# Kernel tuning notes

Hardware: AMD Instinct MI355X
Metric: run time of the kernel (lower is better)

## Reference

```python
import jax, jax.numpy as jnp
import numpy as np

B, S, H = 8, 2048, 1024  # batch, sqi_dim, hidden_dim


def setup_inputs() -> dict:
    key = jax.random.key(0)
    ks = jax.random.split(key, 10)
    lim_h = 1.0 / np.sqrt(H)
    lim_1 = 1.0  # Linear(1, H): fan_in = 1
    return {
        "hidden_states": jax.random.normal(ks[0], (B, S, H), dtype=jnp.float32),
        "sqi_sequence": jax.random.uniform(ks[1], (B, 1, S), dtype=jnp.float32),
        "pos_enc": jnp.zeros((1, S, H), dtype=jnp.float32),
        "Wq": jax.random.uniform(ks[2], (H, H), minval=-lim_h, maxval=lim_h),
        "bq": jax.random.uniform(ks[3], (H,), minval=-lim_h, maxval=lim_h),
        "Wk": jax.random.uniform(ks[4], (H, 1), minval=-lim_1, maxval=lim_1),
        "bk": jax.random.uniform(ks[5], (H,), minval=-lim_1, maxval=lim_1),
        "Wv": jax.random.uniform(ks[6], (H, H), minval=-lim_h, maxval=lim_h),
        "bv": jax.random.uniform(ks[7], (H,), minval=-lim_h, maxval=lim_h),
    }


def reference(hidden_states, sqi_sequence, pos_enc, Wq, bq, Wk, bk, Wv, bv):
    # hidden_states: [B, S, H]; sqi_sequence: [B, 1, S]
    x = hidden_states + pos_enc[:, :S, :]
    q = jnp.einsum("bsh,oh->bso", x, Wq) + bq                     # [B, S, H]
    sqi = jnp.transpose(sqi_sequence, (0, 2, 1))                   # [B, S, 1]
    k = sqi * Wk[:, 0] + bk                                        # Linear(1->H): [B, S, H]
    v = jnp.einsum("bsh,oh->bso", x, Wv) + bv                     # [B, S, H]
    scores = jnp.einsum("bqh,bkh->bqk", q, k) / jnp.sqrt(jnp.float32(H))
    attn = jax.nn.softmax(scores, axis=-1)                         # dropout = identity (eval)
    out = jnp.einsum("bqk,bkh->bqh", attn, v)                      # [B, S, H]
    context = jnp.mean(out, axis=1)                                # [B, H]
    return context, attn
```

## Files before the change

### kernel.cpp

```cpp
#include <hip/hip_runtime.h>
#include <math.h>

#define Bq 8
#define Sq 2048
#define Hq 1024
#define QT 8
#define INV_SQRT_H (1.0f / 32.0f)

typedef float f32x4 __attribute__((ext_vector_type(4)));

__device__ __forceinline__ float waveReduceSum(float v) {
#pragma unroll
    for (int off = 32; off > 0; off >>= 1) v += __shfl_xor(v, off, 64);
    return v;
}

__global__ void k_prep(const float* __restrict__ Wq, const float* __restrict__ Wk,
                       const float* __restrict__ bq, const float* __restrict__ sqi,
                       float* __restrict__ wq_eff, float* __restrict__ cb,
                       float* __restrict__ ext) {
    int bid = blockIdx.x, t = threadIdx.x;
    int wid = t >> 6, lane = t & 63;
    if (bid < 256) {
        int hc = bid & 3, oc = bid >> 2;
        int h = hc * 256 + t, o0 = oc * 16;
        float acc = 0.f;
#pragma unroll
        for (int o = 0; o < 16; ++o)
            acc += Wq[(size_t)(o0 + o) * Hq + h] * Wk[o0 + o];
        atomicAdd(&wq_eff[h], acc);
    } else if (bid == 256) {
        float acc = 0.f;
#pragma unroll
        for (int j = 0; j < 4; ++j) acc += bq[t * 4 + j] * Wk[t * 4 + j];
        acc = waveReduceSum(acc);
        __shared__ float red[4];
        if (lane == 0) red[wid] = acc;
        __syncthreads();
        if (t == 0) *cb = (red[0] + red[1] + red[2] + red[3]) * INV_SQRT_H;
    } else {
        int b = bid - 257;
        float mn = 1e30f, mx = -1e30f;
        for (int j = t; j < Sq; j += 256) {
            float v = sqi[b * Sq + j];
            mn = fminf(mn, v);
            mx = fmaxf(mx, v);
        }
#pragma unroll
        for (int off = 32; off > 0; off >>= 1) {
            mn = fminf(mn, __shfl_xor(mn, off, 64));
            mx = fmaxf(mx, __shfl_xor(mx, off, 64));
        }
        __shared__ float smn[4], smx[4];
        if (lane == 0) { smn[wid] = mn; smx[wid] = mx; }
        __syncthreads();
        if (t == 0) {
            ext[b]      = fminf(fminf(smn[0], smn[1]), fminf(smn[2], smn[3]));
            ext[Bq + b] = fmaxf(fmaxf(smx[0], smx[1]), fmaxf(smx[2], smx[3]));
        }
    }
}

__global__ void __launch_bounds__(256) k_attn(
        const float* __restrict__ hidden, const float* __restrict__ pos,
        const float* __restrict__ wq_eff, const float* __restrict__ cbp,
        const float* __restrict__ sqi, const float* __restrict__ ext,
        float* __restrict__ attn, float* __restrict__ wcol) {
    int b = blockIdx.y, qt = blockIdx.x, t = threadIdx.x;
    int wid = t >> 6, lane = t & 63;
    __shared__ float sqi_s[Sq];
    __shared__ float colsum[Sq];
    {
        const float4* sp = (const float4*)(sqi + b * Sq);
        float4* ds = (float4*)sqi_s;
        ds[t]       = sp[t];
        ds[256 + t] = sp[256 + t];
        float4* cz = (float4*)colsum;
        cz[t]       = make_float4(0.f, 0.f, 0.f, 0.f);
        cz[256 + t] = make_float4(0.f, 0.f, 0.f, 0.f);
    }
    float smin = ext[b], smax = ext[Bq + b];
    float cbv = *cbp;

    const float4* wp = (const float4*)wq_eff;
    float4 w0 = wp[lane], w1 = wp[lane + 64], w2 = wp[lane + 128], w3 = wp[lane + 192];
    int q0 = qt * QT + wid * 2;
    float a[2];
#pragma unroll
    for (int r = 0; r < 2; ++r) {
        const float4* hp = (const float4*)(hidden + (size_t)(b * Sq + q0 + r) * Hq);
        const float4* pp = (const float4*)(pos + (size_t)(q0 + r) * Hq);
        float4 h0 = hp[lane], h1 = hp[lane + 64], h2 = hp[lane + 128], h3 = hp[lane + 192];
        float4 p0 = pp[lane], p1 = pp[lane + 64], p2 = pp[lane + 128], p3 = pp[lane + 192];
        float d = (h0.x + p0.x) * w0.x + (h0.y + p0.y) * w0.y + (h0.z + p0.z) * w0.z + (h0.w + p0.w) * w0.w
                + (h1.x + p1.x) * w1.x + (h1.y + p1.y) * w1.y + (h1.z + p1.z) * w1.z + (h1.w + p1.w) * w1.w
                + (h2.x + p2.x) * w2.x + (h2.y + p2.y) * w2.y + (h2.z + p2.z) * w2.z + (h2.w + p2.w) * w2.w
                + (h3.x + p3.x) * w3.x + (h3.y + p3.y) * w3.y + (h3.z + p3.z) * w3.z + (h3.w + p3.w) * w3.w;
        d = waveReduceSum(d);
        a[r] = d * INV_SQRT_H + cbv;
    }
    __syncthreads();

    const float4* ss = (const float4*)sqi_s;
    float4 ca[8];
#pragma unroll
    for (int c = 0; c < 8; ++c) ca[c] = make_float4(0.f, 0.f, 0.f, 0.f);

#pragma unroll
    for (int r = 0; r < 2; ++r) {
        float aa = a[r];
        float m = (aa > 0.f) ? aa * smax : aa * smin;
        float4 e[8];
        float s = 0.f;
#pragma unroll
        for (int c = 0; c < 8; ++c) {
            float4 sv = ss[lane + 64 * c];
            e[c].x = __expf(aa * sv.x - m);
            e[c].y = __expf(aa * sv.y - m);
            e[c].z = __expf(aa * sv.z - m);
            e[c].w = __expf(aa * sv.w - m);
            s += e[c].x + e[c].y + e[c].z + e[c].w;
        }
        s = waveReduceSum(s);
        float rinv = 1.0f / s;
        f32x4* orow = (f32x4*)(attn + (size_t)(b * Sq + q0 + r) * Sq);
#pragma unroll
        for (int c = 0; c < 8; ++c) {
            f32x4 p;
            p.x = e[c].x * rinv; p.y = e[c].y * rinv;
            p.z = e[c].z * rinv; p.w = e[c].w * rinv;
            __builtin_nontemporal_store(p, &orow[lane + 64 * c]);
            ca[c].x += p.x; ca[c].y += p.y; ca[c].z += p.z; ca[c].w += p.w;
        }
    }

#pragma unroll
    for (int c = 0; c < 8; ++c) {
        int base = (lane + 64 * c) * 4;
        atomicAdd(&colsum[base + 0], ca[c].x);
        atomicAdd(&colsum[base + 1], ca[c].y);
        atomicAdd(&colsum[base + 2], ca[c].z);
        atomicAdd(&colsum[base + 3], ca[c].w);
    }
    __syncthreads();
#pragma unroll
    for (int j = 0; j < 8; ++j)
        atomicAdd(&wcol[b * Sq + j * 256 + t], colsum[j * 256 + t]);
}

__global__ void k_y(const float* __restrict__ hidden, const float* __restrict__ pos,
                    const float* __restrict__ wcol, float* __restrict__ y) {
    int b = blockIdx.y, kc = blockIdx.x, t = threadIdx.x;
    int kk0 = kc * 32;
    float4 acc = {0, 0, 0, 0};
#pragma unroll 8
    for (int i = 0; i < 32; ++i) {
        int kk = kk0 + i;
        float wv = wcol[b * Sq + kk] * (1.0f / Sq);
        float4 hv = ((const float4*)(hidden + ((size_t)(b * Sq + kk)) * Hq))[t];
        float4 pv = ((const float4*)(pos + (size_t)kk * Hq))[t];
        acc.x += wv * (hv.x + pv.x);
        acc.y += wv * (hv.y + pv.y);
        acc.z += wv * (hv.z + pv.z);
        acc.w += wv * (hv.w + pv.w);
    }
    atomicAdd(&y[b * Hq + t * 4 + 0], acc.x);
    atomicAdd(&y[b * Hq + t * 4 + 1], acc.y);
    atomicAdd(&y[b * Hq + t * 4 + 2], acc.z);
    atomicAdd(&y[b * Hq + t * 4 + 3], acc.w);
}

__global__ void k_ctx(const float* __restrict__ Wv, const float* __restrict__ bv,
                      const float* __restrict__ y, float* __restrict__ ctx) {
    int b = blockIdx.y, t = threadIdx.x;
    int wid = t >> 6, lane = t & 63;
    __shared__ float4 ys4[Hq / 4];
    ys4[t] = ((const float4*)(y + b * Hq))[t];
    __syncthreads();
    float4 y0 = ys4[lane], y1 = ys4[lane + 64], y2 = ys4[lane + 128], y3 = ys4[lane + 192];
    int h0 = blockIdx.x * 16 + wid * 4;
#pragma unroll
    for (int r = 0; r < 4; ++r) {
        int h = h0 + r;
        const float4* wrow = (const float4*)(Wv + (size_t)h * Hq);
        float4 v0 = wrow[lane], v1 = wrow[lane + 64], v2 = wrow[lane + 128], v3 = wrow[lane + 192];
        float d = v0.x * y0.x + v0.y * y0.y + v0.z * y0.z + v0.w * y0.w
                + v1.x * y1.x + v1.y * y1.y + v1.z * y1.z + v1.w * y1.w
                + v2.x * y2.x + v2.y * y2.y + v2.z * y2.z + v2.w * y2.w
                + v3.x * y3.x + v3.y * y3.y + v3.z * y3.z + v3.w * y3.w;
        d = waveReduceSum(d);
        if (lane == 0) ctx[b * Hq + h] = d + bv[h];
    }
}

extern "C" void kernel_launch(void* const* d_in, const int* in_sizes, int n_in,
                              void* d_out, int out_size, void* d_ws, size_t ws_size,
                              hipStream_t stream) {
    const float* hidden = (const float*)d_in[0];
    const float* sqi    = (const float*)d_in[1];
    const float* pos    = (const float*)d_in[2];
    const float* Wq     = (const float*)d_in[3];
    const float* bq     = (const float*)d_in[4];
    const float* Wk     = (const float*)d_in[5];
    const float* Wv     = (const float*)d_in[7];
    const float* bv     = (const float*)d_in[8];

    float* out  = (float*)d_out;
    float* ctx  = out;
    float* attn = out + Bq * Hq;

    float* ws     = (float*)d_ws;
    float* wq_eff = ws;
    float* wcol   = ws + 1024;
    float* y      = ws + 17408;
    float* ext    = ws + 25600;
    float* cb     = ws + 25616;

    (void)hipMemsetAsync(ws, 0, 25600 * sizeof(float), stream);

    k_prep<<<265, 256, 0, stream>>>(Wq, Wk, bq, sqi, wq_eff, cb, ext);
    k_attn<<<dim3(Sq / QT, Bq), 256, 0, stream>>>(hidden, pos, wq_eff, cb,
                                                  sqi, ext, attn, wcol);
    k_y   <<<dim3(64, Bq), 256, 0, stream>>>(hidden, pos, wcol, y);
    k_ctx <<<dim3(Hq / 16, Bq), 256, 0, stream>>>(Wv, bv, y, ctx);
}
```

Measured before the change: 307.6 us.

## Split attention into row-stats, column-sum, and pure-write kernels

Splits the fused attention kernel into three. The first computes each row's score scale and softmax normaliser. The second recomputes the exponentials in column order to form the column sums of attn without shared or global atomics per element. The third recomputes the probabilities and only streams the attn matrix out, with 16 rows per block. This removes the per-block shared-memory atomic column reduction and lets the write kernel be purely bandwidth-bound. In exchange it adds extra kernel launches and recomputes the exponentials twice more, including a 512-iteration serial loop per thread in the column-sum kernel.

```diff
diff --git a/kernel.cpp b/kernel.cpp
--- a/kernel.cpp
+++ b/kernel.cpp
@@ -4,7 +4,7 @@
 #define Bq 8
 #define Sq 2048
 #define Hq 1024
-#define QT 8
+#define QT 16
 #define INV_SQRT_H (1.0f / 32.0f)
 
 typedef float f32x4 __attribute__((ext_vector_type(4)));
@@ -13,6 +13,10 @@
 #pragma unroll
     for (int off = 32; off > 0; off >>= 1) v += __shfl_xor(v, off, 64);
     return v;
+}
+
+__device__ __forceinline__ float rowMax(float aa, float smin, float smax) {
+    return fmaxf(aa * smax, aa * smin);
 }
 
 __global__ void k_prep(const float* __restrict__ Wq, const float* __restrict__ Wk,
@@ -61,91 +65,120 @@
     }
 }
 
-__global__ void __launch_bounds__(256) k_attn(
+__global__ void __launch_bounds__(256) k_a(
         const float* __restrict__ hidden, const float* __restrict__ pos,
         const float* __restrict__ wq_eff, const float* __restrict__ cbp,
         const float* __restrict__ sqi, const float* __restrict__ ext,
-        float* __restrict__ attn, float* __restrict__ wcol) {
-    int b = blockIdx.y, qt = blockIdx.x, t = threadIdx.x;
+        float* __restrict__ a_arr, float* __restrict__ rinv_arr) {
+    int b = blockIdx.y, t = threadIdx.x;
     int wid = t >> 6, lane = t & 63;
     __shared__ float sqi_s[Sq];
-    __shared__ float colsum[Sq];
     {
         const float4* sp = (const float4*)(sqi + b * Sq);
         float4* ds = (float4*)sqi_s;
         ds[t]       = sp[t];
         ds[256 + t] = sp[256 + t];
-        float4* cz = (float4*)colsum;
-        cz[t]       = make_float4(0.f, 0.f, 0.f, 0.f);
-        cz[256 + t] = make_float4(0.f, 0.f, 0.f, 0.f);
     }
     float smin = ext[b], smax = ext[Bq + b];
     float cbv = *cbp;
 
+    int q = blockIdx.x * 4 + wid;
+    const float4* hp = (const float4*)(hidden + (size_t)(b * Sq + q) * Hq);
+    const float4* pp = (const float4*)(pos + (size_t)q * Hq);
     const float4* wp = (const float4*)wq_eff;
-    float4 w0 = wp[lane], w1 = wp[lane + 64], w2 = wp[lane + 128], w3 = wp[lane + 192];
-    int q0 = qt * QT + wid * 2;
-    float a[2];
-#pragma unroll
-    for (int r = 0; r < 2; ++r) {
-        const float4* hp = (const float4*)(hidden + (size_t)(b * Sq + q0 + r) * Hq);
-        const float4* pp = (const float4*)(pos + (size_t)(q0 + r) * Hq);
-        float4 h0 = hp[lane], h1 = hp[lane + 64], h2 = hp[lane + 128], h3 = hp[lane + 192];
-        float4 p0 = pp[lane], p1 = pp[lane + 64], p2 = pp[lane + 128], p3 = pp[lane + 192];
-        float d = (h0.x + p0.x) * w0.x + (h0.y + p0.y) * w0.y + (h0.z + p0.z) * w0.z + (h0.w + p0.w) * w0.w
-                + (h1.x + p1.x) * w1.x + (h1.y + p1.y) * w1.y + (h1.z + p1.z) * w1.z + (h1.w + p1.w) * w1.w
-                + (h2.x + p2.x) * w2.x + (h2.y + p2.y) * w2.y + (h2.z + p2.z) * w2.z + (h2.w + p2.w) * w2.w
-                + (h3.x + p3.x) * w3.x + (h3.y + p3.y) * w3.y + (h3.z + p3.z) * w3.z + (h3.w + p3.w) * w3.w;
-        d = waveReduceSum(d);
-        a[r] = d * INV_SQRT_H + cbv;
-    }
+    float d = 0.f;
+#pragma unroll
+    for (int seg = 0; seg < 4; ++seg) {
+        float4 h = hp[lane + 64 * seg];
+        float4 p = pp[lane + 64 * seg];
+        float4 w = wp[lane + 64 * seg];
+        d += (h.x + p.x) * w.x + (h.y + p.y) * w.y +
+             (h.z + p.z) * w.z + (h.w + p.w) * w.w;
+    }
+    d = waveReduceSum(d);
+    float aa = d * INV_SQRT_H + cbv;
+    float m = rowMax(aa, smin, smax);
     __syncthreads();
 
     const float4* ss = (const float4*)sqi_s;
-    float4 ca[8];
-#pragma unroll
-    for (int c = 0; c < 8; ++c) ca[c] = make_float4(0.f, 0.f, 0.f, 0.f);
-
-#pragma unroll
-    for (int r = 0; r < 2; ++r) {
-        float aa = a[r];
-        float m = (aa > 0.f) ? aa * smax : aa * smin;
-        float4 e[8];
-        float s = 0.f;
+    float s = 0.f;
+#pragma unroll
+    for (int c = 0; c < 8; ++c) {
+        float4 sv = ss[lane + 64 * c];
+        s += __expf(aa * sv.x - m) + __expf(aa * sv.y - m)
+           + __expf(aa * sv.z - m) + __expf(aa * sv.w - m);
+    }
+    s = waveReduceSum(s);
+    if (lane == 0) {
+        a_arr[b * Sq + q]    = aa;
+        rinv_arr[b * Sq + q] = 1.0f / s;
+    }
+}
+
+__global__ void __launch_bounds__(256) k_wcol(
+        const float* __restrict__ sqi, const float* __restrict__ a_arr,
+        const float* __restrict__ rinv_arr, const float* __restrict__ ext,
+        float* __restrict__ wcol) {
+    int b = blockIdx.y;
+    int kt = blockIdx.x >> 2;
+    int qc = blockIdx.x & 3;
+    int t = threadIdx.x;
+    __shared__ float a_s[512], r_s[512];
+    int qbase = qc * 512;
+    a_s[t]       = a_arr[b * Sq + qbase + t];
+    a_s[256 + t] = a_arr[b * Sq + qbase + 256 + t];
+    r_s[t]       = rinv_arr[b * Sq + qbase + t];
+    r_s[256 + t] = rinv_arr[b * Sq + qbase + 256 + t];
+    float smin = ext[b], smax = ext[Bq + b];
+    int kk = kt * 256 + t;
+    float sk = sqi[b * Sq + kk];
+    __syncthreads();
+    float acc = 0.f;
+#pragma unroll 4
+    for (int j = 0; j < 512; ++j) {
+        float aa = a_s[j];
+        float m = rowMax(aa, smin, smax);
+        acc += r_s[j] * __expf(aa * sk - m);
+    }
+    atomicAdd(&wcol[b * Sq + kk], acc);
+}
+
+__global__ void __launch_bounds__(256) k_attn_w(
+        const float* __restrict__ sqi, const float* __restrict__ a_arr,
+        const float* __restrict__ rinv_arr, const float* __restrict__ ext,
+        float* __restrict__ attn) {
+    int b = blockIdx.y, qt = blockIdx.x, t = threadIdx.x;
+    int wid = t >> 6, lane = t & 63;
+    __shared__ float sqi_s[Sq];
+    {
+        const float4* sp = (const float4*)(sqi + b * Sq);
+        float4* ds = (float4*)sqi_s;
+        ds[t]       = sp[t];
+        ds[256 + t] = sp[256 + t];
+    }
+    float smin = ext[b], smax = ext[Bq + b];
+    __syncthreads();
+
+    const float4* ss = (const float4*)sqi_s;
+    int q0 = qt * QT + wid * (QT / 4);
+#pragma unroll
+    for (int r = 0; r < QT / 4; ++r) {
+        int q = q0 + r;
+        float aa = a_arr[b * Sq + q];
+        float rv = rinv_arr[b * Sq + q];
+        float m = rowMax(aa, smin, smax);
+        f32x4* orow = (f32x4*)(attn + (size_t)(b * Sq + q) * Sq);
 #pragma unroll
         for (int c = 0; c < 8; ++c) {
             float4 sv = ss[lane + 64 * c];
-            e[c].x = __expf(aa * sv.x - m);
-            e[c].y = __expf(aa * sv.y - m);
-            e[c].z = __expf(aa * sv.z - m);
-            e[c].w = __expf(aa * sv.w - m);
-            s += e[c].x + e[c].y + e[c].z + e[c].w;
-        }
-        s = waveReduceSum(s);
-        float rinv = 1.0f / s;
-        f32x4* orow = (f32x4*)(attn + (size_t)(b * Sq + q0 + r) * Sq);
-#pragma unroll
-        for (int c = 0; c < 8; ++c) {
             f32x4 p;
-            p.x = e[c].x * rinv; p.y = e[c].y * rinv;
-            p.z = e[c].z * rinv; p.w = e[c].w * rinv;
+            p.x = __expf(aa * sv.x - m) * rv;
+            p.y = __expf(aa * sv.y - m) * rv;
+            p.z = __expf(aa * sv.z - m) * rv;
+            p.w = __expf(aa * sv.w - m) * rv;
             __builtin_nontemporal_store(p, &orow[lane + 64 * c]);
-            ca[c].x += p.x; ca[c].y += p.y; ca[c].z += p.z; ca[c].w += p.w;
-        }
-    }
-
-#pragma unroll
-    for (int c = 0; c < 8; ++c) {
-        int base = (lane + 64 * c) * 4;
-        atomicAdd(&colsum[base + 0], ca[c].x);
-        atomicAdd(&colsum[base + 1], ca[c].y);
-        atomicAdd(&colsum[base + 2], ca[c].z);
-        atomicAdd(&colsum[base + 3], ca[c].w);
-    }
-    __syncthreads();
-#pragma unroll
-    for (int j = 0; j < 8; ++j)
-        atomicAdd(&wcol[b * Sq + j * 256 + t], colsum[j * 256 + t]);
+        }
+    }
 }
 
 __global__ void k_y(const float* __restrict__ hidden, const float* __restrict__ pos,
@@ -209,18 +242,22 @@
     float* ctx  = out;
     float* attn = out + Bq * Hq;
 
-    float* ws     = (float*)d_ws;
-    float* wq_eff = ws;
-    float* wcol   = ws + 1024;
-    float* y      = ws + 17408;
-    float* ext    = ws + 25600;
-    float* cb     = ws + 25616;
+    float* ws       = (float*)d_ws;
+    float* wq_eff   = ws;
+    float* wcol     = ws + 1024;
+    float* y        = ws + 17408;
+    float* ext      = ws + 25600;
+    float* cb       = ws + 25616;
+    float* a_arr    = ws + 25632;
+    float* rinv_arr = ws + 42016;
 
     (void)hipMemsetAsync(ws, 0, 25600 * sizeof(float), stream);
 
-    k_prep<<<265, 256, 0, stream>>>(Wq, Wk, bq, sqi, wq_eff, cb, ext);
-    k_attn<<<dim3(Sq / QT, Bq), 256, 0, stream>>>(hidden, pos, wq_eff, cb,
-                                                  sqi, ext, attn, wcol);
-    k_y   <<<dim3(64, Bq), 256, 0, stream>>>(hidden, pos, wcol, y);
-    k_ctx <<<dim3(Hq / 16, Bq), 256, 0, stream>>>(Wv, bv, y, ctx);
-}
+    k_prep  <<<265, 256, 0, stream>>>(Wq, Wk, bq, sqi, wq_eff, cb, ext);
+    k_a     <<<dim3(Sq / 4, Bq), 256, 0, stream>>>(hidden, pos, wq_eff, cb,
+                                                   sqi, ext, a_arr, rinv_arr);
+    k_wcol  <<<dim3(32, Bq), 256, 0, stream>>>(sqi, a_arr, rinv_arr, ext, wcol);
+    k_attn_w<<<dim3(Sq / QT, Bq), 256, 0, stream>>>(sqi, a_arr, rinv_arr, ext, attn);
+    k_y     <<<dim3(64, Bq), 256, 0, stream>>>(hidden, pos, wcol, y);
+    k_ctx   <<<dim3(Hq / 16, Bq), 256, 0, stream>>>(Wv, bv, y, ctx);
+}
```

After: 259.4 us. -15.7%, faster.
